# Optimization experiments

Measured on AMD Instinct MI355X. Metric: run time of the kernel, lower is better.

## Reference

```python
import jax, jax.numpy as jnp
import numpy as np

N, K, D = 32768, 4096, 256


def setup_inputs() -> dict:
    key = jax.random.key(0)
    k1, k2 = jax.random.split(key)
    z_e = jax.random.normal(k1, (N, D), dtype=jnp.float32)
    embed = jax.random.normal(k2, (K, D), dtype=jnp.float32)
    return {"z_e": z_e, "embed": embed}


def reference(z_e, embed):
    # squared L2 distances: ||z||^2 - 2 z.E^T + ||e||^2  -> [N, K]
    d = (jnp.sum(z_e * z_e, axis=1, keepdims=True)
         - 2.0 * (z_e @ embed.T)
         + jnp.sum(embed * embed, axis=1))
    idx = jnp.argmin(d, axis=1)                      # [N] int32
    one_hot = jax.nn.one_hot(idx, K, dtype=z_e.dtype)  # [N, K]
    z_q = one_hot @ embed                            # [N, D] (matches torch's one_hot @ embed)
    return (z_q, idx, one_hot)
```

## Files before the change

kernel.cpp:

```cpp
#include <hip/hip_runtime.h>


#define N_TOK 32768
#define K_CODE 4096
#define D_DIM 256
#define BM 64

typedef float f32x4 __attribute__((ext_vector_type(4)));
typedef short s16x8 __attribute__((ext_vector_type(8)));
typedef int   i32x4 __attribute__((ext_vector_type(4)));

#define OUT_FLOATS 142639104u
#define SCR_FLOATS 1576960u
#define SCR_OFF    (OUT_FLOATS - SCR_FLOATS)
#define EFRAG_SHORTS (3u * K_CODE * D_DIM)

static __device__ __forceinline__ unsigned short f2bf(float f) {
    unsigned int u = __float_as_uint(f);
    u = (u + 0x7fffu + ((u >> 16) & 1u)) >> 16;
    return (unsigned short)u;
}
static __device__ __forceinline__ float bf2f(unsigned short b) {
    return __uint_as_float(((unsigned int)b) << 16);
}

__global__ __launch_bounds__(256) void vq_prep(const float* __restrict__ embed,
                                               float* __restrict__ out) {
    __shared__ float part[8][33];
    unsigned short* escr = (unsigned short*)(out + SCR_OFF);
    float* e2g = out + SCR_OFF + (EFRAG_SHORTS / 2);

    const int t    = threadIdx.x;
    const int cl   = t >> 5;
    const int r32  = t & 31;
    const int dc   = r32 >> 2;
    const int quad = r32 & 3;
    const int k    = blockIdx.x * 8 + cl;

    const float* src = embed + (size_t)k * D_DIM + dc * 32 + quad * 8;
    float x[8];
    *(float4*)(x)     = *(const float4*)(src);
    *(float4*)(x + 4) = *(const float4*)(src + 4);

    s16x8 hv, mv, lv;
    float s2 = 0.0f;
#pragma unroll
    for (int j = 0; j < 8; ++j) {
        const float xx = x[j];
        s2 += xx * xx;
        const unsigned short bh = f2bf(xx);
        const float r1 = xx - bf2f(bh);
        const unsigned short bm = f2bf(r1);
        const float r2 = r1 - bf2f(bm);
        const unsigned short bl = f2bf(r2);
        hv[j] = (short)bh; mv[j] = (short)bm; lv[j] = (short)bl;
    }

    const int ct_g = k >> 4;
    const int lane = quad * 16 + (k & 15);
    const size_t base = ((size_t)(ct_g * 8 + dc) * 3) * 512 + lane * 8;
    *(s16x8*)&escr[base]         = hv;
    *(s16x8*)&escr[base + 512]   = mv;
    *(s16x8*)&escr[base + 1024]  = lv;

    part[cl][r32] = s2;
    __syncthreads();
    if (t < 8) {
        float s = 0.0f;
#pragma unroll
        for (int j = 0; j < 32; ++j) s += part[t][j];
        e2g[blockIdx.x * 8 + t] = s;
    }
}

__global__ __launch_bounds__(512, 2)
void vq_argmin_mfma(const float* __restrict__ z_e, float* __restrict__ out) {
    __shared__ __align__(16) short As[49152];
    __shared__ __align__(16) short Bs[24576];
    __shared__ float e2s[256];
    __shared__ float redv[64][4];
    __shared__ int   redi[64][4];

    const unsigned short* escr = (const unsigned short*)(out + SCR_OFF);
    const float* e2g = out + SCR_OFF + (EFRAG_SHORTS / 2);

    const int t    = threadIdx.x;
    const int w    = t >> 6;
    const int wr   = w >> 2;
    const int wc   = w & 3;
    const int lane = t & 63;
    const int n    = lane & 15;
    const int quad = lane >> 4;
    const int row0 = blockIdx.x * BM;

#pragma unroll
    for (int i = 0; i < 4; ++i) {
        const int run  = t + 512 * i;
        const int qs   = run & 3;
        const int dcs  = (run >> 2) & 7;
        const int row  = run >> 5;
        const float* src = z_e + (size_t)(row0 + row) * D_DIM + dcs * 32 + qs * 8;
        float x[8];
        *(float4*)(x)     = *(const float4*)(src);
        *(float4*)(x + 4) = *(const float4*)(src + 4);
        s16x8 hv, mv, lv;
#pragma unroll
        for (int j = 0; j < 8; ++j) {
            const float xx = x[j];
            const unsigned short bh = f2bf(xx);
            const float r1 = xx - bf2f(bh);
            const unsigned short bm = f2bf(r1);
            const float r2 = r1 - bf2f(bm);
            hv[j] = (short)bh; mv[j] = (short)bm; lv[j] = (short)f2bf(r2);
        }
        const int rtile = row >> 4;
        const int ls    = qs * 16 + (row & 15);
        *(s16x8*)&As[((0 * 4 + rtile) * 8 + dcs) * 512 + ls * 8] = hv;
        *(s16x8*)&As[((1 * 4 + rtile) * 8 + dcs) * 512 + ls * 8] = mv;
        *(s16x8*)&As[((2 * 4 + rtile) * 8 + dcs) * 512 + ls * 8] = lv;
    }

    float bv[8];
    int   bidx[8];
#pragma unroll
    for (int s = 0; s < 8; ++s) { bv[s] = 3.0e38f; bidx[s] = 0; }

#pragma unroll 1
    for (int kt = 0; kt < 16; ++kt) {
        const int kc = kt * 256;
        __syncthreads();
        if (t < 256) e2s[t] = e2g[kc + t];

        f32x4 acc[2][4];
#pragma unroll
        for (int rt = 0; rt < 2; ++rt)
#pragma unroll
            for (int u = 0; u < 4; ++u) acc[rt][u] = (f32x4){0.f, 0.f, 0.f, 0.f};

#pragma unroll 1
        for (int dc = 0; dc < 8; ++dc) {
            if (dc) __syncthreads();
#pragma unroll
            for (int s = 0; s < 6; ++s) {
                const int chunk = t + 512 * s;
                const int frag  = chunk >> 6;
                const int lf    = chunk & 63;
                const int c     = frag >> 4;
                const int ctile = frag & 15;
                const int ct_g  = (kc >> 4) + ctile;
                const i32x4 v = *(const i32x4*)&escr[((size_t)(ct_g * 8 + dc) * 3 + c) * 512 + lf * 8];
                *(i32x4*)&Bs[(c * 16 + ctile) * 512 + lf * 8] = v;
            }
            __syncthreads();

            s16x8 af[2][3], bfm[4][3];
#pragma unroll
            for (int rt = 0; rt < 2; ++rt)
#pragma unroll
                for (int c = 0; c < 3; ++c)
                    af[rt][c] = *(const s16x8*)&As[((c * 4 + wr * 2 + rt) * 8 + dc) * 512 + lane * 8];
#pragma unroll
            for (int u = 0; u < 4; ++u)
#pragma unroll
                for (int c = 0; c < 3; ++c)
                    bfm[u][c] = *(const s16x8*)&Bs[(c * 16 + wc * 4 + u) * 512 + lane * 8];

#pragma unroll
            for (int rt = 0; rt < 2; ++rt)
#pragma unroll
                for (int u = 0; u < 4; ++u) {
                    f32x4 a = acc[rt][u];
                    a = __builtin_amdgcn_mfma_f32_16x16x32_bf16(af[rt][0], bfm[u][0], a, 0, 0, 0);
                    a = __builtin_amdgcn_mfma_f32_16x16x32_bf16(af[rt][0], bfm[u][1], a, 0, 0, 0);
                    a = __builtin_amdgcn_mfma_f32_16x16x32_bf16(af[rt][1], bfm[u][0], a, 0, 0, 0);
                    a = __builtin_amdgcn_mfma_f32_16x16x32_bf16(af[rt][1], bfm[u][1], a, 0, 0, 0);
                    a = __builtin_amdgcn_mfma_f32_16x16x32_bf16(af[rt][0], bfm[u][2], a, 0, 0, 0);
                    a = __builtin_amdgcn_mfma_f32_16x16x32_bf16(af[rt][2], bfm[u][0], a, 0, 0, 0);
                    acc[rt][u] = a;
                }
        }

#pragma unroll
        for (int u = 0; u < 4; ++u) {
            const int   code = kc + wc * 64 + u * 16 + n;
            const float e2v  = e2s[wc * 64 + u * 16 + n];
#pragma unroll
            for (int rt = 0; rt < 2; ++rt)
#pragma unroll
                for (int r = 0; r < 4; ++r) {
                    const float val = fmaf(-2.0f, acc[rt][u][r], e2v);
                    const int slot = rt * 4 + r;
                    if (val < bv[slot]) { bv[slot] = val; bidx[slot] = code; }
                }
        }
    }

#pragma unroll
    for (int slot = 0; slot < 8; ++slot) {
#pragma unroll
        for (int mask = 1; mask < 16; mask <<= 1) {
            const float ov = __shfl_xor(bv[slot], mask);
            const int   oi = __shfl_xor(bidx[slot], mask);
            if (ov < bv[slot] || (ov == bv[slot] && oi < bidx[slot])) {
                bv[slot] = ov; bidx[slot] = oi;
            }
        }
    }
    if (n == 0) {
#pragma unroll
        for (int rt = 0; rt < 2; ++rt)
#pragma unroll
            for (int r = 0; r < 4; ++r) {
                const int row_local = wr * 32 + rt * 16 + quad * 4 + r;
                redv[row_local][wc] = bv[rt * 4 + r];
                redi[row_local][wc] = bidx[rt * 4 + r];
            }
    }
    __syncthreads();
    if (t < 64) {
        float v = redv[t][0];
        int  bi = redi[t][0];
#pragma unroll
        for (int j = 1; j < 4; ++j) {
            const float v2 = redv[t][j];
            const int   i2 = redi[t][j];
            if (v2 < v || (v2 == v && i2 < bi)) { v = v2; bi = i2; }
        }
        out[(size_t)N_TOK * D_DIM + (size_t)(row0 + t)] = (float)bi;
    }
}

__launch_bounds__(256, 2)
__global__ void vq_epilogue(const float* __restrict__ embed,
                            float* __restrict__ out) {
    __shared__ int bks[32];
    const int t    = threadIdx.x;
    const int w    = t >> 6;
    const int lane = t & 63;
    const int row0 = blockIdx.x * 32;

    const float* idxf = out + (size_t)N_TOK * D_DIM;
    float* zq = out;
    float* oh = out + (size_t)N_TOK * D_DIM + N_TOK;

    if (t < 32) bks[t] = (int)idxf[row0 + t];
    __syncthreads();

#pragma unroll 1
    for (int rr = 0; rr < 8; ++rr) {
        const int r   = rr * 4 + w;
        const int row = row0 + r;
        const int bk  = bks[r];

        f32x4 v = *(const f32x4*)&embed[(size_t)bk * D_DIM + lane * 4];
        __builtin_nontemporal_store(v, (f32x4*)&zq[(size_t)row * D_DIM + lane * 4]);

        float* ohrow = &oh[(size_t)row * K_CODE];
#pragma unroll
        for (int g = 0; g < 16; ++g) {
            const int base = (g * 64 + lane) * 4;
            f32x4 u;
            u.x = (bk == base    ) ? 1.0f : 0.0f;
            u.y = (bk == base + 1) ? 1.0f : 0.0f;
            u.z = (bk == base + 2) ? 1.0f : 0.0f;
            u.w = (bk == base + 3) ? 1.0f : 0.0f;
            __builtin_nontemporal_store(u, (f32x4*)&ohrow[base]);
        }
    }
}

extern "C" void kernel_launch(void* const* d_in, const int* in_sizes, int n_in,
                              void* d_out, int out_size, void* d_ws, size_t ws_size,
                              hipStream_t stream) {
    const float* z_e   = (const float*)d_in[0];
    const float* embed = (const float*)d_in[1];
    float* out = (float*)d_out;

    hipLaunchKernelGGL(vq_prep,        dim3(K_CODE / 8),  dim3(256), 0, stream, embed, out);
    hipLaunchKernelGGL(vq_argmin_mfma, dim3(N_TOK / BM),  dim3(512), 0, stream, z_e, out);
    hipLaunchKernelGGL(vq_epilogue,    dim3(N_TOK / 32),  dim3(256), 0, stream, embed, out);
}
```

Measured before the change: 992.3 us.

## Load codebook fragments directly from global memory, dropping shared B staging

The argmin kernel stops staging codebook fragments through shared memory with per-chunk barriers. Each of the 8 waves now owns 32 codes per K tile and covers all 64 rows, reading its B fragments straight from global/L2 and e2 directly from global. This removes the inner-loop syncthreads and LDS writes, but every block re-reads the codebook from cache without sharing it across waves, and each thread keeps more accumulators. The epilogue also switches to smaller blocks with higher occupancy bounds.

```diff
diff --git a/kernel.cpp b/kernel.cpp
--- a/kernel.cpp
+++ b/kernel.cpp
@@ -52,16 +52,15 @@
         const float r1 = xx - bf2f(bh);
         const unsigned short bm = f2bf(r1);
         const float r2 = r1 - bf2f(bm);
-        const unsigned short bl = f2bf(r2);
-        hv[j] = (short)bh; mv[j] = (short)bm; lv[j] = (short)bl;
+        hv[j] = (short)bh; mv[j] = (short)bm; lv[j] = (short)f2bf(r2);
     }
 
     const int ct_g = k >> 4;
     const int lane = quad * 16 + (k & 15);
     const size_t base = ((size_t)(ct_g * 8 + dc) * 3) * 512 + lane * 8;
-    *(s16x8*)&escr[base]         = hv;
-    *(s16x8*)&escr[base + 512]   = mv;
-    *(s16x8*)&escr[base + 1024]  = lv;
+    *(s16x8*)&escr[base]        = hv;
+    *(s16x8*)&escr[base + 512]  = mv;
+    *(s16x8*)&escr[base + 1024] = lv;
 
     part[cl][r32] = s2;
     __syncthreads();
@@ -76,18 +75,14 @@
 __global__ __launch_bounds__(512, 2)
 void vq_argmin_mfma(const float* __restrict__ z_e, float* __restrict__ out) {
     __shared__ __align__(16) short As[49152];
-    __shared__ __align__(16) short Bs[24576];
-    __shared__ float e2s[256];
-    __shared__ float redv[64][4];
-    __shared__ int   redi[64][4];
+    __shared__ float redv[64][9];
+    __shared__ int   redi[64][9];
 
     const unsigned short* escr = (const unsigned short*)(out + SCR_OFF);
     const float* e2g = out + SCR_OFF + (EFRAG_SHORTS / 2);
 
     const int t    = threadIdx.x;
     const int w    = t >> 6;
-    const int wr   = w >> 2;
-    const int wc   = w & 3;
     const int lane = t & 63;
     const int n    = lane & 15;
     const int quad = lane >> 4;
@@ -110,8 +105,7 @@
             const unsigned short bh = f2bf(xx);
             const float r1 = xx - bf2f(bh);
             const unsigned short bm = f2bf(r1);
-            const float r2 = r1 - bf2f(bm);
-            hv[j] = (short)bh; mv[j] = (short)bm; lv[j] = (short)f2bf(r2);
+            hv[j] = (short)bh; mv[j] = (short)bm; lv[j] = (short)f2bf(r1 - bf2f(bm));
         }
         const int rtile = row >> 4;
         const int ls    = qs * 16 + (row & 15);
@@ -119,73 +113,56 @@
         *(s16x8*)&As[((1 * 4 + rtile) * 8 + dcs) * 512 + ls * 8] = mv;
         *(s16x8*)&As[((2 * 4 + rtile) * 8 + dcs) * 512 + ls * 8] = lv;
     }
-
-    float bv[8];
-    int   bidx[8];
-#pragma unroll
-    for (int s = 0; s < 8; ++s) { bv[s] = 3.0e38f; bidx[s] = 0; }
+    __syncthreads();
+
+    float bv[16];
+    int   bidx[16];
+#pragma unroll
+    for (int s = 0; s < 16; ++s) { bv[s] = 3.0e38f; bidx[s] = 0; }
 
 #pragma unroll 1
     for (int kt = 0; kt < 16; ++kt) {
-        const int kc = kt * 256;
-        __syncthreads();
-        if (t < 256) e2s[t] = e2g[kc + t];
-
-        f32x4 acc[2][4];
-#pragma unroll
-        for (int rt = 0; rt < 2; ++rt)
-#pragma unroll
-            for (int u = 0; u < 4; ++u) acc[rt][u] = (f32x4){0.f, 0.f, 0.f, 0.f};
+        f32x4 acc[4][2];
+#pragma unroll
+        for (int rt = 0; rt < 4; ++rt)
+#pragma unroll
+            for (int u = 0; u < 2; ++u) acc[rt][u] = (f32x4){0.f, 0.f, 0.f, 0.f};
 
 #pragma unroll 1
         for (int dc = 0; dc < 8; ++dc) {
-            if (dc) __syncthreads();
-#pragma unroll
-            for (int s = 0; s < 6; ++s) {
-                const int chunk = t + 512 * s;
-                const int frag  = chunk >> 6;
-                const int lf    = chunk & 63;
-                const int c     = frag >> 4;
-                const int ctile = frag & 15;
-                const int ct_g  = (kc >> 4) + ctile;
-                const i32x4 v = *(const i32x4*)&escr[((size_t)(ct_g * 8 + dc) * 3 + c) * 512 + lf * 8];
-                *(i32x4*)&Bs[(c * 16 + ctile) * 512 + lf * 8] = v;
-            }
-            __syncthreads();
-
-            s16x8 af[2][3], bfm[4][3];
-#pragma unroll
-            for (int rt = 0; rt < 2; ++rt)
+            s16x8 bfm[2][3];
+#pragma unroll
+            for (int u = 0; u < 2; ++u) {
+                const int ct_g = kt * 16 + w * 2 + u;
 #pragma unroll
                 for (int c = 0; c < 3; ++c)
-                    af[rt][c] = *(const s16x8*)&As[((c * 4 + wr * 2 + rt) * 8 + dc) * 512 + lane * 8];
-#pragma unroll
-            for (int u = 0; u < 4; ++u)
-#pragma unroll
-                for (int c = 0; c < 3; ++c)
-                    bfm[u][c] = *(const s16x8*)&Bs[(c * 16 + wc * 4 + u) * 512 + lane * 8];
-
-#pragma unroll
-            for (int rt = 0; rt < 2; ++rt)
-#pragma unroll
-                for (int u = 0; u < 4; ++u) {
+                    bfm[u][c] = *(const s16x8*)&escr[((size_t)(ct_g * 8 + dc) * 3 + c) * 512 + lane * 8];
+            }
+#pragma unroll
+            for (int rt = 0; rt < 4; ++rt) {
+                s16x8 af0 = *(const s16x8*)&As[((0 * 4 + rt) * 8 + dc) * 512 + lane * 8];
+                s16x8 af1 = *(const s16x8*)&As[((1 * 4 + rt) * 8 + dc) * 512 + lane * 8];
+                s16x8 af2 = *(const s16x8*)&As[((2 * 4 + rt) * 8 + dc) * 512 + lane * 8];
+#pragma unroll
+                for (int u = 0; u < 2; ++u) {
                     f32x4 a = acc[rt][u];
-                    a = __builtin_amdgcn_mfma_f32_16x16x32_bf16(af[rt][0], bfm[u][0], a, 0, 0, 0);
-                    a = __builtin_amdgcn_mfma_f32_16x16x32_bf16(af[rt][0], bfm[u][1], a, 0, 0, 0);
-                    a = __builtin_amdgcn_mfma_f32_16x16x32_bf16(af[rt][1], bfm[u][0], a, 0, 0, 0);
-                    a = __builtin_amdgcn_mfma_f32_16x16x32_bf16(af[rt][1], bfm[u][1], a, 0, 0, 0);
-                    a = __builtin_amdgcn_mfma_f32_16x16x32_bf16(af[rt][0], bfm[u][2], a, 0, 0, 0);
-                    a = __builtin_amdgcn_mfma_f32_16x16x32_bf16(af[rt][2], bfm[u][0], a, 0, 0, 0);
+                    a = __builtin_amdgcn_mfma_f32_16x16x32_bf16(af0, bfm[u][0], a, 0, 0, 0);
+                    a = __builtin_amdgcn_mfma_f32_16x16x32_bf16(af0, bfm[u][1], a, 0, 0, 0);
+                    a = __builtin_amdgcn_mfma_f32_16x16x32_bf16(af1, bfm[u][0], a, 0, 0, 0);
+                    a = __builtin_amdgcn_mfma_f32_16x16x32_bf16(af1, bfm[u][1], a, 0, 0, 0);
+                    a = __builtin_amdgcn_mfma_f32_16x16x32_bf16(af0, bfm[u][2], a, 0, 0, 0);
+                    a = __builtin_amdgcn_mfma_f32_16x16x32_bf16(af2, bfm[u][0], a, 0, 0, 0);
                     acc[rt][u] = a;
                 }
-        }
-
-#pragma unroll
-        for (int u = 0; u < 4; ++u) {
-            const int   code = kc + wc * 64 + u * 16 + n;
-            const float e2v  = e2s[wc * 64 + u * 16 + n];
-#pragma unroll
-            for (int rt = 0; rt < 2; ++rt)
+            }
+        }
+
+#pragma unroll
+        for (int u = 0; u < 2; ++u) {
+            const int  code = kt * 256 + (w * 2 + u) * 16 + n;
+            const float e2v = e2g[code];
+#pragma unroll
+            for (int rt = 0; rt < 4; ++rt)
 #pragma unroll
                 for (int r = 0; r < 4; ++r) {
                     const float val = fmaf(-2.0f, acc[rt][u][r], e2v);
@@ -196,7 +173,7 @@
     }
 
 #pragma unroll
-    for (int slot = 0; slot < 8; ++slot) {
+    for (int slot = 0; slot < 16; ++slot) {
 #pragma unroll
         for (int mask = 1; mask < 16; mask <<= 1) {
             const float ov = __shfl_xor(bv[slot], mask);
@@ -208,12 +185,12 @@
     }
     if (n == 0) {
 #pragma unroll
-        for (int rt = 0; rt < 2; ++rt)
+        for (int rt = 0; rt < 4; ++rt)
 #pragma unroll
             for (int r = 0; r < 4; ++r) {
-                const int row_local = wr * 32 + rt * 16 + quad * 4 + r;
-                redv[row_local][wc] = bv[rt * 4 + r];
-                redi[row_local][wc] = bidx[rt * 4 + r];
+                const int row_local = rt * 16 + quad * 4 + r;
+                redv[row_local][w] = bv[rt * 4 + r];
+                redi[row_local][w] = bidx[rt * 4 + r];
             }
     }
     __syncthreads();
@@ -221,7 +198,7 @@
         float v = redv[t][0];
         int  bi = redi[t][0];
 #pragma unroll
-        for (int j = 1; j < 4; ++j) {
+        for (int j = 1; j < 8; ++j) {
             const float v2 = redv[t][j];
             const int   i2 = redi[t][j];
             if (v2 < v || (v2 == v && i2 < bi)) { v = v2; bi = i2; }
@@ -230,24 +207,24 @@
     }
 }
 
-__launch_bounds__(256, 2)
+__launch_bounds__(256, 8)
 __global__ void vq_epilogue(const float* __restrict__ embed,
                             float* __restrict__ out) {
-    __shared__ int bks[32];
+    __shared__ int bks[16];
     const int t    = threadIdx.x;
     const int w    = t >> 6;
     const int lane = t & 63;
-    const int row0 = blockIdx.x * 32;
+    const int row0 = blockIdx.x * 16;
 
     const float* idxf = out + (size_t)N_TOK * D_DIM;
     float* zq = out;
     float* oh = out + (size_t)N_TOK * D_DIM + N_TOK;
 
-    if (t < 32) bks[t] = (int)idxf[row0 + t];
+    if (t < 16) bks[t] = (int)idxf[row0 + t];
     __syncthreads();
 
 #pragma unroll 1
-    for (int rr = 0; rr < 8; ++rr) {
+    for (int rr = 0; rr < 4; ++rr) {
         const int r   = rr * 4 + w;
         const int row = row0 + r;
         const int bk  = bks[r];
@@ -276,7 +253,7 @@
     const float* embed = (const float*)d_in[1];
     float* out = (float*)d_out;
 
-    hipLaunchKernelGGL(vq_prep,        dim3(K_CODE / 8),  dim3(256), 0, stream, embed, out);
-    hipLaunchKernelGGL(vq_argmin_mfma, dim3(N_TOK / BM),  dim3(512), 0, stream, z_e, out);
-    hipLaunchKernelGGL(vq_epilogue,    dim3(N_TOK / 32),  dim3(256), 0, stream, embed, out);
-}
+    hipLaunchKernelGGL(vq_prep,        dim3(K_CODE / 8), dim3(256), 0, stream, embed, out);
+    hipLaunchKernelGGL(vq_argmin_mfma, dim3(N_TOK / BM), dim3(512), 0, stream, z_e, out);
+    hipLaunchKernelGGL(vq_epilogue,    dim3(N_TOK / 16), dim3(256), 0, stream, embed, out);
+}
```

New measurement: 874.1 us. 11.9% less time.
